# Performance work log

Hardware: AMD Instinct MI355X
Metric: run time of the kernel (lower is better)

## Reference

```python
import jax, jax.numpy as jnp
import numpy as np

PF_DIM = 1024
F_DIM = 1024
LOW = 128
MID = 32  # low_dim // 4
BATCH = 8192


def setup_inputs() -> dict:
    key = jax.random.key(0)
    ks = jax.random.split(key, 10)
    s = lambda fan_in: 1.0 / np.sqrt(fan_in)
    return {
        "f": jax.random.normal(ks[0], (BATCH, F_DIM), jnp.float32),
        "pf": jax.random.normal(ks[1], (BATCH, PF_DIM), jnp.float32),
        # nn.Linear weights are (out, in)
        "proj_f_w": jax.random.uniform(ks[2], (LOW, F_DIM), jnp.float32, -s(F_DIM), s(F_DIM)),
        "proj_f_b": jax.random.uniform(ks[3], (LOW,), jnp.float32, -s(F_DIM), s(F_DIM)),
        "proj_pf_w": jax.random.uniform(ks[4], (LOW, PF_DIM), jnp.float32, -s(PF_DIM), s(PF_DIM)),
        "proj_pf_b": jax.random.uniform(ks[5], (LOW,), jnp.float32, -s(PF_DIM), s(PF_DIM)),
        "proj_f2_w": jax.random.uniform(ks[6], (F_DIM, LOW), jnp.float32, -s(LOW), s(LOW)),
        "proj_f2_b": jax.random.uniform(ks[7], (F_DIM,), jnp.float32, -s(LOW), s(LOW)),
        "pg_w": jax.random.uniform(ks[8], (2 * LOW * MID, LOW), jnp.float32, -s(LOW), s(LOW)),
        "pg_b": jax.random.uniform(ks[9], (2 * LOW * MID,), jnp.float32, -s(LOW), s(LOW)),
    }


def reference(f, pf, proj_f_w, proj_f_b, proj_pf_w, proj_pf_b,
              proj_f2_w, proj_f2_b, pg_w, pg_b):
    b = pf.shape[0]
    # project both inputs to low_dim
    f_low = f @ proj_f_w.T + proj_f_b              # (b, LOW)
    pf_low = pf @ proj_pf_w.T + proj_pf_b          # (b, LOW)
    # per-sample generated weights
    params = pf_low @ pg_w.T + pg_b                # (b, 2*LOW*MID)
    dim = LOW * MID
    p1 = params[:, :dim].reshape(b, LOW, MID)      # (b, LOW, MID)
    p2 = params[:, dim:].reshape(b, MID, LOW)      # (b, MID, LOW)
    # batched tiny MLP: (b,1,LOW)@(b,LOW,MID) -> relu -> @(b,MID,LOW)
    h = jax.nn.relu(jnp.einsum('bl,blm->bm', f_low, p1))
    g = jnp.einsum('bm,bml->bl', h, p2)            # (b, LOW)
    out = g @ proj_f2_w.T + proj_f2_b + f + pf     # (b, F_DIM)
    return out
```

## Files before the change

kernel.cpp:

```cpp
#include <hip/hip_runtime.h>
#include <stdint.h>


typedef __attribute__((ext_vector_type(8))) short bf16x8;
typedef __attribute__((ext_vector_type(4))) float f32x4;

#define MFMA(a, b, c) __builtin_amdgcn_mfma_f32_16x16x32_bf16((a), (b), (c), 0, 0, 0)

__device__ __forceinline__ ushort f2bf(float x) {
    union { float f; uint32_t u; } v; v.f = x;
    return (ushort)((v.u + 0x7FFFu + ((v.u >> 16) & 1u)) >> 16);
}
__device__ __forceinline__ ushort4 f2bf4(float4 v) {
    ushort4 o; o.x = f2bf(v.x); o.y = f2bf(v.y); o.z = f2bf(v.z); o.w = f2bf(v.w); return o;
}
__device__ __forceinline__ float bf2f(ushort u) {
    union { uint32_t i; float f; } v; v.i = ((uint32_t)u) << 16; return v.f;
}

__global__ __launch_bounds__(256) void k0_convert(
    const float* __restrict__ pgw, const float* __restrict__ wf,
    const float* __restrict__ wpf, const float* __restrict__ w2,
    ushort* __restrict__ pg_img, ushort* __restrict__ w_img, ushort* __restrict__ w2_img)
{
    int cid = blockIdx.x * 256 + threadIdx.x;
    const float* src; ushort* dst;
    if (cid < 131072) {
        int lane = cid & 63, ks = (cid >> 6) & 3, T = cid >> 8;
        int j = T * 16 + (lane & 15), k = ks * 32 + (lane >> 4) * 8;
        src = pgw + (size_t)j * 128 + k;
        dst = pg_img + (size_t)cid * 8;
    } else if (cid < 163840) {
        int c = cid - 131072;
        int lane = c & 63, ks = (c >> 6) & 31, lt = (c >> 11) & 7, mat = c >> 14;
        int l = lt * 16 + (lane & 15), k = ks * 32 + (lane >> 4) * 8;
        src = (mat ? wpf : wf) + (size_t)l * 1024 + k;
        dst = w_img + (size_t)c * 8;
    } else {
        int c = cid - 163840;
        int lane = c & 63, ks = (c >> 6) & 3, nt = c >> 8;
        int n = nt * 16 + (lane & 15), k = ks * 32 + (lane >> 4) * 8;
        src = w2 + (size_t)n * 128 + k;
        dst = w2_img + (size_t)c * 8;
    }
    float4 a = ((const float4*)src)[0], b = ((const float4*)src)[1];
    ((ushort4*)dst)[0] = f2bf4(a);
    ((ushort4*)dst)[1] = f2bf4(b);
}

__global__ __launch_bounds__(256, 1) void mega(
    const float* __restrict__ f, const float* __restrict__ pf,
    const ushort* __restrict__ w_img, const float* __restrict__ bfb,
    const float* __restrict__ bpfb, const ushort* __restrict__ pg_img,
    const float* __restrict__ pgb, const ushort* __restrict__ w2_img,
    const float* __restrict__ b2, float* __restrict__ out)
{
    __shared__ __align__(16) char smem[62464];
    ushort* As    = (ushort*)smem;
    ushort* Tr    = (ushort*)smem;
    float*  hred  = (float*)smem;
    float*  hl    = (float*)(smem + 16384);
    float*  gred  = (float*)smem;
    float*  Ls    = (float*)smem;
    ushort* flowT = (ushort*)(smem + 36864);
    ushort* pfrag = (ushort*)(smem + 46080);
    ushort* gfrag = (ushort*)(smem + 54272);

    const int tid = threadIdx.x;
    const int lane = tid & 63, wid = tid >> 6;
    const int q = lane >> 4, r15 = lane & 15;
    const int b0 = blockIdx.x * 32;

#pragma unroll 1
    for (int mat = 0; mat < 2; mat++) {
        const float* src = mat ? pf : f;
        const float* bias_ptr = mat ? bpfb : bfb;
        float bias_v[2];
#pragma unroll
        for (int j = 0; j < 2; j++) bias_v[j] = bias_ptr[wid * 32 + j * 16 + r15];

        f32x4 c[2][2];
        c[0][0] = c[0][1] = c[1][0] = c[1][1] = (f32x4){0.f, 0.f, 0.f, 0.f};

#pragma unroll 1
        for (int kh = 0; kh < 2; kh++) {
            __syncthreads();
#pragma unroll
            for (int half = 0; half < 2; half++) {
                float4 v[8];
#pragma unroll
                for (int rr = 0; rr < 8; rr++) {
                    int row = (half * 8 + rr) * 2 + (tid >> 7);
                    v[rr] = *(const float4*)(src + (size_t)(b0 + row) * 1024 + kh * 512 + (tid & 127) * 4);
                }
#pragma unroll
                for (int rr = 0; rr < 8; rr++) {
                    int row = (half * 8 + rr) * 2 + (tid >> 7);
                    *(ushort4*)(As + row * 520 + (tid & 127) * 4) = f2bf4(v[rr]);
                }
            }
            __syncthreads();
            const int lt0 = wid * 2;
#pragma unroll
            for (int ks = 0; ks < 16; ks++) {
                bf16x8 w0 = *(const bf16x8*)(w_img + (size_t)mat * 131072 + ((size_t)(lt0 + 0) * 32 + kh * 16 + ks) * 512 + lane * 8);
                bf16x8 w1 = *(const bf16x8*)(w_img + (size_t)mat * 131072 + ((size_t)(lt0 + 1) * 32 + kh * 16 + ks) * 512 + lane * 8);
                bf16x8 a0 = *(const bf16x8*)(As + (0 * 16 + r15) * 520 + ks * 32 + q * 8);
                bf16x8 a1 = *(const bf16x8*)(As + (1 * 16 + r15) * 520 + ks * 32 + q * 8);
                c[0][0] = MFMA(a0, w0, c[0][0]);
                c[0][1] = MFMA(a0, w1, c[0][1]);
                c[1][0] = MFMA(a1, w0, c[1][0]);
                c[1][1] = MFMA(a1, w1, c[1][1]);
            }
        }
        if (mat == 0) {
#pragma unroll
            for (int mt = 0; mt < 2; mt++)
#pragma unroll
                for (int j = 0; j < 2; j++) {
                    int l = wid * 32 + j * 16 + r15;
#pragma unroll
                    for (int r = 0; r < 4; r++)
                        flowT[l * 36 + mt * 16 + q * 4 + r] = f2bf(c[mt][j][r] + bias_v[j]);
                }
        } else {
            __syncthreads();
#pragma unroll
            for (int mt = 0; mt < 2; mt++)
#pragma unroll
                for (int j = 0; j < 2; j++) {
                    int l = wid * 32 + j * 16 + r15;
#pragma unroll
                    for (int r = 0; r < 4; r++)
                        Tr[(mt * 16 + q * 4 + r) * 136 + l] = f2bf(c[mt][j][r] + bias_v[j]);
                }
            __syncthreads();
#pragma unroll
            for (int pass = 0; pass < 2; pass++) {
                int chunkid = pass * 4 + (tid >> 6);
                int bt = chunkid >> 2, ks2 = chunkid & 3;
                int ln = tid & 63;
                int k0 = ks2 * 32 + (ln >> 4) * 8;
                uint4 tv = *(const uint4*)(Tr + (bt * 16 + (ln & 15)) * 136 + k0);
                *(uint4*)(pfrag + (size_t)chunkid * 512 + ln * 8) = tv;
            }
        }
    }
    __syncthreads();

    bf16x8 bfr[2][4];
#pragma unroll
    for (int ct = 0; ct < 2; ct++)
#pragma unroll
        for (int ks = 0; ks < 4; ks++)
            bfr[ct][ks] = *(const bf16x8*)(pfrag + (size_t)(ct * 4 + ks) * 512 + lane * 8);

    f32x4 hacc[2][2];
    hacc[0][0] = hacc[0][1] = hacc[1][0] = hacc[1][1] = (f32x4){0.f, 0.f, 0.f, 0.f};

#pragma unroll 1
    for (int jg = 0; jg < 8; jg++) {
        const ushort* Tbase = pg_img + (size_t)(jg * 32 + wid * 8) * 2048;
        bf16x8 af[2][4];
#pragma unroll
        for (int ks = 0; ks < 4; ks++) af[0][ks] = *(const bf16x8*)(Tbase + ks * 512 + lane * 8);
#pragma unroll
        for (int i = 0; i < 8; i++) {
            const int cur = i & 1, nxt = cur ^ 1;
            if (i < 7) {
#pragma unroll
                for (int ks = 0; ks < 4; ks++)
                    af[nxt][ks] = *(const bf16x8*)(Tbase + (size_t)(i + 1) * 2048 + ks * 512 + lane * 8);
            }
            const int tl = wid * 8 + i;
            const int mh = tl & 1;
            f32x4 bv = *(const f32x4*)(pgb + (size_t)(jg * 32 + tl) * 16 + q * 4);
            const int fbase = (jg * 16 + (tl >> 1)) * 36;
#pragma unroll
            for (int ct = 0; ct < 2; ct++) {
                f32x4 cc = (f32x4){0.f, 0.f, 0.f, 0.f};
#pragma unroll
                for (int ks = 0; ks < 4; ks++) cc = MFMA(af[cur][ks], bfr[ct][ks], cc);
                float s = bf2f(flowT[fbase + ct * 16 + r15]);
#pragma unroll
                for (int r = 0; r < 4; r++) hacc[mh][ct][r] += s * (cc[r] + bv[r]);
            }
        }
    }
#pragma unroll
    for (int mh = 0; mh < 2; mh++)
#pragma unroll
        for (int ct = 0; ct < 2; ct++)
#pragma unroll
            for (int r = 0; r < 4; r++)
                hred[wid * 1024 + (mh * 16 + q * 4 + r) * 32 + ct * 16 + r15] = hacc[mh][ct][r];
    __syncthreads();
    {
        int m = tid >> 3, bq = (tid & 7) * 4;
        const float* h0 = hred + m * 32 + bq;
        float4 s;
        s.x = fmaxf(h0[0] + h0[1024] + h0[2048] + h0[3072], 0.f);
        s.y = fmaxf(h0[1] + h0[1025] + h0[2049] + h0[3073], 0.f);
        s.z = fmaxf(h0[2] + h0[1026] + h0[2050] + h0[3074], 0.f);
        s.w = fmaxf(h0[3] + h0[1027] + h0[2051] + h0[3075], 0.f);
        *(float4*)(hl + m * 32 + bq) = s;
    }
    __syncthreads();

#pragma unroll 1
    for (int lg = 0; lg < 4; lg++) {
        f32x4 gacc[2][2];
        gacc[0][0] = gacc[0][1] = gacc[1][0] = gacc[1][1] = (f32x4){0.f, 0.f, 0.f, 0.f};
        bf16x8 af[2][4];
#pragma unroll
        for (int ks = 0; ks < 4; ks++)
            af[0][ks] = *(const bf16x8*)(pg_img + (size_t)(256 + wid * 8 + lg * 2) * 2048 + ks * 512 + lane * 8);
#pragma unroll
        for (int ti = 0; ti < 16; ti++) {
            const int cur = ti & 1, nxt = cur ^ 1;
            if (ti < 15) {
                const int tn = ti + 1;
                const int mn = wid + 4 * (tn >> 1), ltn = tn & 1;
                const ushort* ap = pg_img + (size_t)(256 + mn * 8 + lg * 2 + ltn) * 2048;
#pragma unroll
                for (int ks = 0; ks < 4; ks++)
                    af[nxt][ks] = *(const bf16x8*)(ap + ks * 512 + lane * 8);
            }
            const int m = wid + 4 * (ti >> 1), lt = ti & 1;
            f32x4 bv = *(const f32x4*)(pgb + 4096 + (size_t)m * 128 + lg * 32 + lt * 16 + q * 4);
#pragma unroll
            for (int ct = 0; ct < 2; ct++) {
                f32x4 cc = (f32x4){0.f, 0.f, 0.f, 0.f};
#pragma unroll
                for (int ks = 0; ks < 4; ks++) cc = MFMA(af[cur][ks], bfr[ct][ks], cc);
                float s = hl[m * 32 + ct * 16 + r15];
#pragma unroll
                for (int r = 0; r < 4; r++) gacc[lt][ct][r] += s * (cc[r] + bv[r]);
            }
        }
#pragma unroll
        for (int lt = 0; lt < 2; lt++)
#pragma unroll
            for (int ct = 0; ct < 2; ct++)
#pragma unroll
                for (int r = 0; r < 4; r++)
                    gred[wid * 1024 + (lt * 16 + q * 4 + r) * 32 + ct * 16 + r15] = gacc[lt][ct][r];
        __syncthreads();
        if (tid < 128) {
            int bt = tid >> 6, ln = tid & 63;
            int b_loc = bt * 16 + (ln & 15);
            int l0 = (ln >> 4) * 8;
            ushort tmp[8];
#pragma unroll
            for (int e = 0; e < 8; e++) {
                const float* gp = gred + (l0 + e) * 32 + b_loc;
                tmp[e] = f2bf(gp[0] + gp[1024] + gp[2048] + gp[3072]);
            }
            ushort4 lo = {tmp[0], tmp[1], tmp[2], tmp[3]};
            ushort4 hi = {tmp[4], tmp[5], tmp[6], tmp[7]};
            ushort* dst = gfrag + (size_t)(bt * 4 + lg) * 512 + ln * 8;
            ((ushort4*)dst)[0] = lo;
            ((ushort4*)dst)[1] = hi;
        }
        __syncthreads();
    }

    bf16x8 afg[2][4];
#pragma unroll
    for (int mtl = 0; mtl < 2; mtl++)
#pragma unroll
        for (int ks = 0; ks < 4; ks++)
            afg[mtl][ks] = *(const bf16x8*)(gfrag + (size_t)(mtl * 4 + ks) * 512 + lane * 8);

#pragma unroll 1
    for (int nb = 0; nb < 4; nb++) {
        float bias_v4[4];
#pragma unroll
        for (int nt = 0; nt < 4; nt++) bias_v4[nt] = b2[nb * 256 + wid * 64 + nt * 16 + r15];
        bf16x8 wfr[2][4];
#pragma unroll
        for (int ks = 0; ks < 4; ks++)
            wfr[0][ks] = *(const bf16x8*)(w2_img + (size_t)((nb * 16 + wid * 4) * 4 + ks) * 512 + lane * 8);
#pragma unroll
        for (int nt = 0; nt < 4; nt++) {
            const int cur = nt & 1, nxt = cur ^ 1;
            if (nt < 3) {
#pragma unroll
                for (int ks = 0; ks < 4; ks++)
                    wfr[nxt][ks] = *(const bf16x8*)(w2_img + (size_t)((nb * 16 + wid * 4 + nt + 1) * 4 + ks) * 512 + lane * 8);
            }
#pragma unroll
            for (int mtl = 0; mtl < 2; mtl++) {
                f32x4 cc = (f32x4){0.f, 0.f, 0.f, 0.f};
#pragma unroll
                for (int ks = 0; ks < 4; ks++) cc = MFMA(afg[mtl][ks], wfr[cur][ks], cc);
                const int nloc = wid * 64 + nt * 16 + r15;
                const int chunk = nloc >> 5, within = nloc & 31;
#pragma unroll
                for (int r = 0; r < 4; r++)
                    Ls[(mtl * 16 + q * 4 + r) * 288 + chunk * 36 + within] = cc[r] + bias_v4[nt];
            }
        }
        __syncthreads();
        {
            const float* ls = Ls + (wid * 8) * 288 + (lane >> 3) * 36 + (lane & 7) * 4;
            const int n0 = nb * 256;
#pragma unroll
            for (int rr = 0; rr < 8; rr++) {
                const int b = b0 + wid * 8 + rr;
                const size_t gbase = (size_t)b * 1024 + n0 + lane * 4;
                float4 lv = *(const float4*)(ls + rr * 288);
                float4 fa = *(const float4*)(f + gbase);
                float4 pa = *(const float4*)(pf + gbase);
                float4 o;
                o.x = lv.x + fa.x + pa.x; o.y = lv.y + fa.y + pa.y;
                o.z = lv.z + fa.z + pa.z; o.w = lv.w + fa.w + pa.w;
                *(float4*)(out + gbase) = o;
            }
        }
        __syncthreads();
    }
}

extern "C" void kernel_launch(void* const* d_in, const int* in_sizes, int n_in,
                              void* d_out, int out_size, void* d_ws, size_t ws_size,
                              hipStream_t stream)
{
    const float* f    = (const float*)d_in[0];
    const float* pf   = (const float*)d_in[1];
    const float* wf   = (const float*)d_in[2];
    const float* bfb  = (const float*)d_in[3];
    const float* wpf  = (const float*)d_in[4];
    const float* bpfb = (const float*)d_in[5];
    const float* w2   = (const float*)d_in[6];
    const float* b2   = (const float*)d_in[7];
    const float* pgw  = (const float*)d_in[8];
    const float* pgb  = (const float*)d_in[9];

    char* ws = (char*)d_ws;
    ushort* pg_img = (ushort*)(ws + 0);
    ushort* w_img  = (ushort*)(ws + 2097152);
    ushort* w2_img = (ushort*)(ws + 2621440);
    float*  out    = (float*)d_out;

    k0_convert<<<dim3(704), dim3(256), 0, stream>>>(pgw, wf, wpf, w2, pg_img, w_img, w2_img);
    mega<<<dim3(256), dim3(256), 0, stream>>>(f, pf, w_img, bfb, bpfb,
                                              pg_img, pgb, w2_img, b2, out);
}
```

Baseline: 192.1 us.

## Double mega kernel block to 512 threads and repartition work across eight waves

```diff
diff --git a/kernel.cpp b/kernel.cpp
--- a/kernel.cpp
+++ b/kernel.cpp
@@ -48,7 +48,7 @@
     ((ushort4*)dst)[1] = f2bf4(b);
 }
 
-__global__ __launch_bounds__(256, 1) void mega(
+__global__ __launch_bounds__(512, 2) void mega(
     const float* __restrict__ f, const float* __restrict__ pf,
     const ushort* __restrict__ w_img, const float* __restrict__ bfb,
     const float* __restrict__ bpfb, const ushort* __restrict__ pg_img,
@@ -59,7 +59,7 @@
     ushort* As    = (ushort*)smem;
     ushort* Tr    = (ushort*)smem;
     float*  hred  = (float*)smem;
-    float*  hl    = (float*)(smem + 16384);
+    float*  hl    = (float*)(smem + 32768);
     float*  gred  = (float*)smem;
     float*  Ls    = (float*)smem;
     ushort* flowT = (ushort*)(smem + 36864);
@@ -75,74 +75,65 @@
     for (int mat = 0; mat < 2; mat++) {
         const float* src = mat ? pf : f;
         const float* bias_ptr = mat ? bpfb : bfb;
-        float bias_v[2];
-#pragma unroll
-        for (int j = 0; j < 2; j++) bias_v[j] = bias_ptr[wid * 32 + j * 16 + r15];
-
-        f32x4 c[2][2];
-        c[0][0] = c[0][1] = c[1][0] = c[1][1] = (f32x4){0.f, 0.f, 0.f, 0.f};
+        float bias_v = bias_ptr[wid * 16 + r15];
+
+        f32x4 c[2];
+        c[0] = (f32x4){0.f, 0.f, 0.f, 0.f};
+        c[1] = (f32x4){0.f, 0.f, 0.f, 0.f};
 
 #pragma unroll 1
         for (int kh = 0; kh < 2; kh++) {
             __syncthreads();
-#pragma unroll
-            for (int half = 0; half < 2; half++) {
-                float4 v[8];
-#pragma unroll
-                for (int rr = 0; rr < 8; rr++) {
-                    int row = (half * 8 + rr) * 2 + (tid >> 7);
-                    v[rr] = *(const float4*)(src + (size_t)(b0 + row) * 1024 + kh * 512 + (tid & 127) * 4);
-                }
-#pragma unroll
-                for (int rr = 0; rr < 8; rr++) {
-                    int row = (half * 8 + rr) * 2 + (tid >> 7);
-                    *(ushort4*)(As + row * 520 + (tid & 127) * 4) = f2bf4(v[rr]);
-                }
+            float4 v[8];
+#pragma unroll
+            for (int rr = 0; rr < 8; rr++) {
+                int row = rr * 4 + (tid >> 7);
+                v[rr] = *(const float4*)(src + (size_t)(b0 + row) * 1024 + kh * 512 + (tid & 127) * 4);
+            }
+#pragma unroll
+            for (int rr = 0; rr < 8; rr++) {
+                int row = rr * 4 + (tid >> 7);
+                *(ushort4*)(As + row * 520 + (tid & 127) * 4) = f2bf4(v[rr]);
             }
             __syncthreads();
-            const int lt0 = wid * 2;
+            const ushort* wb = w_img + (size_t)mat * 131072 + ((size_t)wid * 32 + kh * 16) * 512;
+            bf16x8 wfr[4];
+#pragma unroll
+            for (int p = 0; p < 4; p++) wfr[p] = *(const bf16x8*)(wb + (size_t)p * 512 + lane * 8);
 #pragma unroll
             for (int ks = 0; ks < 16; ks++) {
-                bf16x8 w0 = *(const bf16x8*)(w_img + (size_t)mat * 131072 + ((size_t)(lt0 + 0) * 32 + kh * 16 + ks) * 512 + lane * 8);
-                bf16x8 w1 = *(const bf16x8*)(w_img + (size_t)mat * 131072 + ((size_t)(lt0 + 1) * 32 + kh * 16 + ks) * 512 + lane * 8);
-                bf16x8 a0 = *(const bf16x8*)(As + (0 * 16 + r15) * 520 + ks * 32 + q * 8);
-                bf16x8 a1 = *(const bf16x8*)(As + (1 * 16 + r15) * 520 + ks * 32 + q * 8);
-                c[0][0] = MFMA(a0, w0, c[0][0]);
-                c[0][1] = MFMA(a0, w1, c[0][1]);
-                c[1][0] = MFMA(a1, w0, c[1][0]);
-                c[1][1] = MFMA(a1, w1, c[1][1]);
+                const int cur = ks & 3;
+                bf16x8 a0 = *(const bf16x8*)(As + (size_t)r15 * 520 + ks * 32 + q * 8);
+                bf16x8 a1 = *(const bf16x8*)(As + (size_t)(16 + r15) * 520 + ks * 32 + q * 8);
+                c[0] = MFMA(a0, wfr[cur], c[0]);
+                c[1] = MFMA(a1, wfr[cur], c[1]);
+                if (ks + 4 < 16)
+                    wfr[cur] = *(const bf16x8*)(wb + (size_t)(ks + 4) * 512 + lane * 8);
             }
         }
         if (mat == 0) {
 #pragma unroll
-            for (int mt = 0; mt < 2; mt++)
-#pragma unroll
-                for (int j = 0; j < 2; j++) {
-                    int l = wid * 32 + j * 16 + r15;
-#pragma unroll
-                    for (int r = 0; r < 4; r++)
-                        flowT[l * 36 + mt * 16 + q * 4 + r] = f2bf(c[mt][j][r] + bias_v[j]);
-                }
+            for (int mt = 0; mt < 2; mt++) {
+                int l = wid * 16 + r15;
+#pragma unroll
+                for (int r = 0; r < 4; r++)
+                    flowT[l * 36 + mt * 16 + q * 4 + r] = f2bf(c[mt][r] + bias_v);
+            }
         } else {
             __syncthreads();
 #pragma unroll
-            for (int mt = 0; mt < 2; mt++)
-#pragma unroll
-                for (int j = 0; j < 2; j++) {
-                    int l = wid * 32 + j * 16 + r15;
-#pragma unroll
-                    for (int r = 0; r < 4; r++)
-                        Tr[(mt * 16 + q * 4 + r) * 136 + l] = f2bf(c[mt][j][r] + bias_v[j]);
-                }
+            for (int mt = 0; mt < 2; mt++) {
+                int l = wid * 16 + r15;
+#pragma unroll
+                for (int r = 0; r < 4; r++)
+                    Tr[(mt * 16 + q * 4 + r) * 136 + l] = f2bf(c[mt][r] + bias_v);
+            }
             __syncthreads();
-#pragma unroll
-            for (int pass = 0; pass < 2; pass++) {
-                int chunkid = pass * 4 + (tid >> 6);
-                int bt = chunkid >> 2, ks2 = chunkid & 3;
-                int ln = tid & 63;
-                int k0 = ks2 * 32 + (ln >> 4) * 8;
-                uint4 tv = *(const uint4*)(Tr + (bt * 16 + (ln & 15)) * 136 + k0);
-                *(uint4*)(pfrag + (size_t)chunkid * 512 + ln * 8) = tv;
+            {
+                int bt = wid >> 2, ks2 = wid & 3;
+                int k0 = ks2 * 32 + (lane >> 4) * 8;
+                uint4 tv = *(const uint4*)(Tr + (size_t)(bt * 16 + (lane & 15)) * 136 + k0);
+                *(uint4*)(pfrag + (size_t)wid * 512 + lane * 8) = tv;
             }
         }
     }
@@ -160,27 +151,25 @@
 
 #pragma unroll 1
     for (int jg = 0; jg < 8; jg++) {
-        const ushort* Tbase = pg_img + (size_t)(jg * 32 + wid * 8) * 2048;
-        bf16x8 af[2][4];
-#pragma unroll
-        for (int ks = 0; ks < 4; ks++) af[0][ks] = *(const bf16x8*)(Tbase + ks * 512 + lane * 8);
-#pragma unroll
-        for (int i = 0; i < 8; i++) {
-            const int cur = i & 1, nxt = cur ^ 1;
-            if (i < 7) {
-#pragma unroll
-                for (int ks = 0; ks < 4; ks++)
-                    af[nxt][ks] = *(const bf16x8*)(Tbase + (size_t)(i + 1) * 2048 + ks * 512 + lane * 8);
-            }
-            const int tl = wid * 8 + i;
-            const int mh = tl & 1;
+        const ushort* Tbase = pg_img + (size_t)(jg * 32 + wid * 4) * 2048;
+        bf16x8 af[4][4];
+#pragma unroll
+        for (int i = 0; i < 4; i++)
+#pragma unroll
+            for (int ks = 0; ks < 4; ks++)
+                af[i][ks] = *(const bf16x8*)(Tbase + (size_t)i * 2048 + ks * 512 + lane * 8);
+#pragma unroll
+        for (int i = 0; i < 4; i++) {
+            const int tl = wid * 4 + i;
+            const int mh = i & 1;
+            const int l_loc = tl >> 1;
             f32x4 bv = *(const f32x4*)(pgb + (size_t)(jg * 32 + tl) * 16 + q * 4);
-            const int fbase = (jg * 16 + (tl >> 1)) * 36;
+            const int fbase = (jg * 16 + l_loc) * 36;
 #pragma unroll
             for (int ct = 0; ct < 2; ct++) {
                 f32x4 cc = (f32x4){0.f, 0.f, 0.f, 0.f};
 #pragma unroll
-                for (int ks = 0; ks < 4; ks++) cc = MFMA(af[cur][ks], bfr[ct][ks], cc);
+                for (int ks = 0; ks < 4; ks++) cc = MFMA(af[i][ks], bfr[ct][ks], cc);
                 float s = bf2f(flowT[fbase + ct * 16 + r15]);
 #pragma unroll
                 for (int r = 0; r < 4; r++) hacc[mh][ct][r] += s * (cc[r] + bv[r]);
@@ -196,14 +185,15 @@
                 hred[wid * 1024 + (mh * 16 + q * 4 + r) * 32 + ct * 16 + r15] = hacc[mh][ct][r];
     __syncthreads();
     {
-        int m = tid >> 3, bq = (tid & 7) * 4;
-        const float* h0 = hred + m * 32 + bq;
-        float4 s;
-        s.x = fmaxf(h0[0] + h0[1024] + h0[2048] + h0[3072], 0.f);
-        s.y = fmaxf(h0[1] + h0[1025] + h0[2049] + h0[3073], 0.f);
-        s.z = fmaxf(h0[2] + h0[1026] + h0[2050] + h0[3074], 0.f);
-        s.w = fmaxf(h0[3] + h0[1027] + h0[2051] + h0[3075], 0.f);
-        *(float4*)(hl + m * 32 + bq) = s;
+        int m = tid >> 4, bc = (tid & 15) * 2;
+        float s0 = 0.f, s1 = 0.f;
+#pragma unroll
+        for (int w = 0; w < 8; w++) {
+            s0 += hred[w * 1024 + m * 32 + bc];
+            s1 += hred[w * 1024 + m * 32 + bc + 1];
+        }
+        hl[m * 32 + bc]     = fmaxf(s0, 0.f);
+        hl[m * 32 + bc + 1] = fmaxf(s1, 0.f);
     }
     __syncthreads();
 
@@ -211,22 +201,19 @@
     for (int lg = 0; lg < 4; lg++) {
         f32x4 gacc[2][2];
         gacc[0][0] = gacc[0][1] = gacc[1][0] = gacc[1][1] = (f32x4){0.f, 0.f, 0.f, 0.f};
-        bf16x8 af[2][4];
-#pragma unroll
-        for (int ks = 0; ks < 4; ks++)
-            af[0][ks] = *(const bf16x8*)(pg_img + (size_t)(256 + wid * 8 + lg * 2) * 2048 + ks * 512 + lane * 8);
-#pragma unroll
-        for (int ti = 0; ti < 16; ti++) {
-            const int cur = ti & 1, nxt = cur ^ 1;
-            if (ti < 15) {
-                const int tn = ti + 1;
-                const int mn = wid + 4 * (tn >> 1), ltn = tn & 1;
-                const ushort* ap = pg_img + (size_t)(256 + mn * 8 + lg * 2 + ltn) * 2048;
-#pragma unroll
-                for (int ks = 0; ks < 4; ks++)
-                    af[nxt][ks] = *(const bf16x8*)(ap + ks * 512 + lane * 8);
-            }
-            const int m = wid + 4 * (ti >> 1), lt = ti & 1;
+        bf16x8 af[4][4];
+#pragma unroll
+        for (int t = 0; t < 4; t++) {
+            const int m = wid + 8 * (t >> 1), lt = t & 1;
+            const ushort* ap = pg_img + (size_t)(256 + m * 8 + lg * 2 + lt) * 2048;
+#pragma unroll
+            for (int ks = 0; ks < 4; ks++)
+                af[t][ks] = *(const bf16x8*)(ap + ks * 512 + lane * 8);
+        }
+#pragma unroll
+        for (int ti = 0; ti < 8; ti++) {
+            const int cur = ti & 3;
+            const int m = wid + 8 * (ti >> 1), lt = ti & 1;
             f32x4 bv = *(const f32x4*)(pgb + 4096 + (size_t)m * 128 + lg * 32 + lt * 16 + q * 4);
 #pragma unroll
             for (int ct = 0; ct < 2; ct++) {
@@ -236,6 +223,14 @@
                 float s = hl[m * 32 + ct * 16 + r15];
 #pragma unroll
                 for (int r = 0; r < 4; r++) gacc[lt][ct][r] += s * (cc[r] + bv[r]);
+            }
+            if (ti + 4 < 8) {
+                const int tn = ti + 4;
+                const int mn = wid + 8 * (tn >> 1), ltn = tn & 1;
+                const ushort* ap = pg_img + (size_t)(256 + mn * 8 + lg * 2 + ltn) * 2048;
+#pragma unroll
+                for (int ks = 0; ks < 4; ks++)
+                    af[cur][ks] = *(const bf16x8*)(ap + ks * 512 + lane * 8);
             }
         }
 #pragma unroll
@@ -253,8 +248,11 @@
             ushort tmp[8];
 #pragma unroll
             for (int e = 0; e < 8; e++) {
-                const float* gp = gred + (l0 + e) * 32 + b_loc;
-                tmp[e] = f2bf(gp[0] + gp[1024] + gp[2048] + gp[3072]);
+                const float* gp = gred + (size_t)(l0 + e) * 32 + b_loc;
+                float s = 0.f;
+#pragma unroll
+                for (int w = 0; w < 8; w++) s += gp[w * 1024];
+                tmp[e] = f2bf(s);
             }
             ushort4 lo = {tmp[0], tmp[1], tmp[2], tmp[3]};
             ushort4 hi = {tmp[4], tmp[5], tmp[6], tmp[7]};
@@ -274,40 +272,34 @@
 
 #pragma unroll 1
     for (int nb = 0; nb < 4; nb++) {
-        float bias_v4[4];
-#pragma unroll
-        for (int nt = 0; nt < 4; nt++) bias_v4[nt] = b2[nb * 256 + wid * 64 + nt * 16 + r15];
-        bf16x8 wfr[2][4];
-#pragma unroll
-        for (int ks = 0; ks < 4; ks++)
-            wfr[0][ks] = *(const bf16x8*)(w2_img + (size_t)((nb * 16 + wid * 4) * 4 + ks) * 512 + lane * 8);
-#pragma unroll
-        for (int nt = 0; nt < 4; nt++) {
-            const int cur = nt & 1, nxt = cur ^ 1;
-            if (nt < 3) {
-#pragma unroll
-                for (int ks = 0; ks < 4; ks++)
-                    wfr[nxt][ks] = *(const bf16x8*)(w2_img + (size_t)((nb * 16 + wid * 4 + nt + 1) * 4 + ks) * 512 + lane * 8);
-            }
+        float bias_v2[2];
+#pragma unroll
+        for (int nt = 0; nt < 2; nt++) bias_v2[nt] = b2[nb * 256 + wid * 32 + nt * 16 + r15];
+        bf16x8 wfr2[2][4];
+#pragma unroll
+        for (int nt = 0; nt < 2; nt++)
+#pragma unroll
+            for (int ks = 0; ks < 4; ks++)
+                wfr2[nt][ks] = *(const bf16x8*)(w2_img + (size_t)((nb * 16 + wid * 2 + nt) * 4 + ks) * 512 + lane * 8);
+#pragma unroll
+        for (int nt = 0; nt < 2; nt++) {
 #pragma unroll
             for (int mtl = 0; mtl < 2; mtl++) {
                 f32x4 cc = (f32x4){0.f, 0.f, 0.f, 0.f};
 #pragma unroll
-                for (int ks = 0; ks < 4; ks++) cc = MFMA(afg[mtl][ks], wfr[cur][ks], cc);
-                const int nloc = wid * 64 + nt * 16 + r15;
-                const int chunk = nloc >> 5, within = nloc & 31;
+                for (int ks = 0; ks < 4; ks++) cc = MFMA(afg[mtl][ks], wfr2[nt][ks], cc);
 #pragma unroll
                 for (int r = 0; r < 4; r++)
-                    Ls[(mtl * 16 + q * 4 + r) * 288 + chunk * 36 + within] = cc[r] + bias_v4[nt];
+                    Ls[(size_t)(mtl * 16 + q * 4 + r) * 288 + wid * 36 + nt * 16 + r15] = cc[r] + bias_v2[nt];
             }
         }
         __syncthreads();
         {
-            const float* ls = Ls + (wid * 8) * 288 + (lane >> 3) * 36 + (lane & 7) * 4;
+            const float* ls = Ls + (size_t)(wid * 4) * 288 + (lane >> 3) * 36 + (lane & 7) * 4;
             const int n0 = nb * 256;
 #pragma unroll
-            for (int rr = 0; rr < 8; rr++) {
-                const int b = b0 + wid * 8 + rr;
+            for (int rr = 0; rr < 4; rr++) {
+                const int b = b0 + wid * 4 + rr;
                 const size_t gbase = (size_t)b * 1024 + n0 + lane * 4;
                 float4 lv = *(const float4*)(ls + rr * 288);
                 float4 fa = *(const float4*)(f + gbase);
@@ -344,6 +336,6 @@
     float*  out    = (float*)d_out;
 
     k0_convert<<<dim3(704), dim3(256), 0, stream>>>(pgw, wf, wpf, w2, pg_img, w_img, w2_img);
-    mega<<<dim3(256), dim3(256), 0, stream>>>(f, pf, w_img, bfb, bpfb,
+    mega<<<dim3(256), dim3(512), 0, stream>>>(f, pf, w_img, bfb, bpfb,
                                               pg_img, pgb, w2_img, b2, out);
 }
```

After: 180.9 us. 1.06x faster.
